# Performance work log

Measured on AMD Instinct MI355X. Metric: run time of the kernel, lower is better.

Reference implementation:

```python
import jax, jax.numpy as jnp
import numpy as np

# SSD300 common_params
MAP_SIZES = np.array([38, 19, 10, 5, 3, 1])
NUM_BOXES = np.array([4, 6, 6, 6, 4, 4])
NUM_OFFSET = 4
LOC_VAR = 0.1
NUM_CLASSES = 21
NEG_POS_RATIO = 3
_counts = MAP_SIZES ** 2 * NUM_BOXES
LAYER_OFFSETS = np.concatenate([[0], np.cumsum(_counts)])[:6]
TOTAL_ANCHORS = int(_counts.sum())  # 8732

B, MAXGT, SEG_HW = 32, 64, 300


def setup_inputs() -> dict:
    key = jax.random.key(0)
    ks = jax.random.split(key, 6)
    rng = np.random.default_rng(0)
    layer = rng.integers(0, 6, (B, MAXGT))
    pos = rng.integers(0, MAP_SIZES[layer] ** 2)
    dbox = rng.integers(0, NUM_BOXES[layer])
    nvalid = rng.integers(8, MAXGT + 1, (B,))
    live = np.arange(MAXGT)[None, :] < nvalid[:, None]
    layer = np.where(live, layer, -100)  # -100 sentinel terminates per-image list
    idx_batch = jnp.asarray(np.stack([np.zeros_like(layer), layer, pos, dbox], -1), dtype=jnp.int64)
    cls_batch = jnp.asarray(rng.integers(1, NUM_CLASSES, (B, MAXGT)), dtype=jnp.int64)
    return {
        "Loc": jax.random.normal(ks[0], (B, TOTAL_ANCHORS, NUM_OFFSET), jnp.float32),
        "Cls": jax.random.normal(ks[1], (B, TOTAL_ANCHORS, NUM_CLASSES), jnp.float32),
        "Seg": jax.random.normal(ks[2], (B, NUM_CLASSES, SEG_HW, SEG_HW), jnp.float32),
        "gt_box_batch": jax.random.uniform(ks[3], (B, MAXGT, NUM_OFFSET), jnp.float32),
        "df_box_batch": jax.random.uniform(ks[4], (B, MAXGT, NUM_OFFSET), jnp.float32),
        "idx_batch": idx_batch,
        "cls_batch": cls_batch,
        "bat_s": B,
        "mining": 1,
        "seg_label": jax.random.randint(ks[5], (B, SEG_HW, SEG_HW), 0, NUM_CLASSES, jnp.int64),
    }


def _build_targets(idx_batch, cls_batch, gt_box_batch, df_box_batch, mining):
    # Vectorized replacement of the nested scalar-scatter loop.
    layer = idx_batch[..., 1]
    fpos = idx_batch[..., 2]
    dbox = idx_batch[..., 3]
    # original loop breaks at first -100: mask everything after it
    valid = jnp.cumprod((layer != -100).astype(jnp.int32), axis=1).astype(bool)
    lc = jnp.clip(layer, 0, 5)
    offs = jnp.asarray(LAYER_OFFSETS)[lc]
    nb = jnp.asarray(NUM_BOXES)[lc]
    # [B, num_boxes, H, W] permuted to [B, H, W, num_boxes] -> flat = pos*nb + dbox
    flat = offs + fpos * nb + dbox
    flat = jnp.where(valid, flat, TOTAL_ANCHORS)  # dump slot
    bsz = idx_batch.shape[0]
    b_idx = jnp.arange(bsz)[:, None]
    init = -1 if mining else 0
    cls_t = jnp.full((bsz, TOTAL_ANCHORS + 1), init, dtype=jnp.int32)
    cls_t = cls_t.at[b_idx, flat].set(jnp.where(valid, cls_batch.astype(jnp.int32), init))
    delta = (gt_box_batch - df_box_batch) / LOC_VAR
    loc_t = jnp.zeros((bsz, TOTAL_ANCHORS + 1, NUM_OFFSET), jnp.float32)
    loc_t = loc_t.at[b_idx, flat].set(jnp.where(valid[..., None], delta, 0.0))
    return cls_t[:, :TOTAL_ANCHORS], loc_t[:, :TOTAL_ANCHORS]


def _mt_loss(Loc, Cls, Seg, gt_box_batch, df_box_batch, idx_batch, cls_batch, mining, seg_label):
    cls_t, loc_t = _build_targets(idx_batch, cls_batch, gt_box_batch, df_box_batch, mining)
    pos = cls_t > 0
    num_pos = jnp.maximum(pos.sum(), 1).astype(jnp.float32)
    logp = jax.nn.log_softmax(Cls, axis=-1)  # [B,N,C]
    ce = -jnp.take_along_axis(logp, jnp.clip(cls_t, 0, NUM_CLASSES - 1)[..., None].astype(jnp.int32), axis=-1)[..., 0]
    loss_cls_pos = jnp.where(pos, ce, 0.0).sum()
    if mining:
        # hard negative mining: top (3*num_pos_i) background losses per image
        ce_bg = -logp[..., 0]
        neg_cand = cls_t == -1
        scores = jnp.where(neg_cand, ce_bg, -jnp.inf)
        order = jnp.argsort(-scores, axis=1)
        rank = jnp.argsort(order, axis=1)
        num_pos_i = pos.sum(axis=1, keepdims=True)
        num_neg_i = jnp.minimum(NEG_POS_RATIO * num_pos_i, neg_cand.sum(axis=1, keepdims=True))
        sel = neg_cand & (rank < num_neg_i)
        loss_cls_neg = jnp.where(sel, ce_bg, 0.0).sum()
    else:
        # all non-positive anchors are explicit background targets (cls_t == 0)
        loss_cls_neg = jnp.where(~pos, ce, 0.0).sum()
    loss_cls = (loss_cls_pos + loss_cls_neg) / num_pos
    d = Loc - loc_t
    ad = jnp.abs(d)
    sl1 = jnp.where(ad < 1.0, 0.5 * d * d, ad - 0.5)
    loss_loc = jnp.where(pos[..., None], sl1, 0.0).sum() / num_pos
    seg_logp = jax.nn.log_softmax(Seg, axis=1)  # [B,C,H,W]
    seg_ce = -jnp.take_along_axis(seg_logp, seg_label[:, None].astype(jnp.int32), axis=1)[:, 0]
    loss_seg = seg_ce.mean()
    return loss_cls + loss_loc + loss_seg


def reference(Loc, Cls, Seg, gt_box_batch, df_box_batch, idx_batch, cls_batch, bat_s, mining, seg_label):
    return _mt_loss(Loc, Cls, Seg, gt_box_batch, df_box_batch, idx_batch, cls_batch, mining, seg_label)
```

## Files before the change

### kernel.cpp

```cpp
#include <hip/hip_runtime.h>
#include <stdint.h>

#define BATCH 32
#define NA 8732
#define NC 21
#define SHW 90000
#define MAXGT 64
#define NQ (SHW / 4)

#define SLABQ 512
#define NSLAB ((NQ + SLABQ - 1) / SLABQ)
#define NBLK (BATCH * NSLAB)

__constant__ int c_loff[6] = {0, 5776, 7942, 8542, 8692, 8728};
__constant__ int c_lnb[6]  = {4, 6, 6, 6, 4, 4};

__device__ __forceinline__ unsigned f2key(float f) {
    unsigned u = __float_as_uint(f);
    return (u & 0x80000000u) ? ~u : (u | 0x80000000u);
}
__device__ __forceinline__ float key2f(unsigned k) {
    return __uint_as_float((k & 0x80000000u) ? (k ^ 0x80000000u) : ~k);
}

__global__ __launch_bounds__(64) void k_init(float* __restrict__ acc, int* __restrict__ npt,
                                             unsigned* __restrict__ done) {
    int t = threadIdx.x;
    if (t < 8) acc[t] = 0.0f;
    if (t == 8) *npt = 0;
    if (t == 9) *done = 0u;
}

__global__ __launch_bounds__(1024) void k_build(
    const int* __restrict__ idxb, const int* __restrict__ clsb,
    const float* __restrict__ gt, const float* __restrict__ df,
    const float* __restrict__ Loc, const int* __restrict__ mining_p,
    signed char* __restrict__ cls_t, float* __restrict__ acc,
    int* __restrict__ num_pos_i, int* __restrict__ neg_cnt_i,
    int* __restrict__ npt)
{
    const int b = blockIdx.x;
    const int tid = threadIdx.x;
    __shared__ int s_flat[MAXGT];
    __shared__ int s_cls[MAXGT];
    __shared__ float s_delta[MAXGT][4];
    __shared__ int s_nv;
    __shared__ float s_wf[16];
    __shared__ int s_wp[16];
    __shared__ int s_wn[16];

    if (tid < MAXGT) {
        int layer = idxb[(b * MAXGT + tid) * 4 + 1];
        int fpos  = idxb[(b * MAXGT + tid) * 4 + 2];
        int dbox  = idxb[(b * MAXGT + tid) * 4 + 3];
        int fl;
        if (layer == -100) fl = -2;
        else {
            int lc = min(max(layer, 0), 5);
            fl = c_loff[lc] + fpos * c_lnb[lc] + dbox;
        }
        s_flat[tid] = fl;
        s_cls[tid] = clsb[b * MAXGT + tid];
        #pragma unroll
        for (int o = 0; o < 4; o++)
            s_delta[tid][o] = (gt[(b * MAXGT + tid) * 4 + o] - df[(b * MAXGT + tid) * 4 + o]) / 0.1f;
    }
    __syncthreads();
    if (tid == 0) {
        int nv = MAXGT;
        for (int j = 0; j < MAXGT; j++) if (s_flat[j] == -2) { nv = j; break; }
        s_nv = nv;
    }
    __syncthreads();
    const int nv = s_nv;

    int rflat[MAXGT];
    #pragma unroll
    for (int j = 0; j < MAXGT; j++)
        rflat[j] = (j < nv) ? s_flat[j] : -3;

    const int mining = *mining_p;
    const signed char cinit = mining ? (signed char)(-1) : (signed char)0;
    int pos_cnt = 0, neg_cnt = 0;
    float loc_sum = 0.0f;

    for (int a = tid; a < NA; a += 1024) {
        int best = -1;
        #pragma unroll
        for (int j = 0; j < MAXGT; j++)
            best = (rflat[j] == a) ? j : best;
        signed char cv = cinit;
        if (best >= 0) cv = (signed char)s_cls[best];
        cls_t[b * NA + a] = cv;
        if (cv > 0) {
            pos_cnt++;
            const float4 l4 = *reinterpret_cast<const float4*>(Loc + ((size_t)b * NA + a) * 4);
            float lv[4] = {l4.x, l4.y, l4.z, l4.w};
            #pragma unroll
            for (int o = 0; o < 4; o++) {
                float d = lv[o] - s_delta[best][o];
                float ad = fabsf(d);
                loc_sum += (ad < 1.0f) ? (0.5f * d * d) : (ad - 0.5f);
            }
        } else if (cv == -1) {
            neg_cnt++;
        }
    }

    #pragma unroll
    for (int d = 32; d > 0; d >>= 1) {
        loc_sum += __shfl_down(loc_sum, d);
        pos_cnt += __shfl_down(pos_cnt, d);
        neg_cnt += __shfl_down(neg_cnt, d);
    }
    const int lane = tid & 63, wv = tid >> 6;
    if (lane == 0) { s_wf[wv] = loc_sum; s_wp[wv] = pos_cnt; s_wn[wv] = neg_cnt; }
    __syncthreads();
    if (tid == 0) {
        float lf = 0.0f; int pp = 0, nn = 0;
        #pragma unroll
        for (int w = 0; w < 16; w++) { lf += s_wf[w]; pp += s_wp[w]; nn += s_wn[w]; }
        atomicAdd(acc + 2, lf);
        num_pos_i[b] = pp;
        atomicAdd(npt, pp);
        neg_cnt_i[b] = nn;
    }
}

__global__ __launch_bounds__(256) void k_cls(
    const float* __restrict__ Cls, const signed char* __restrict__ cls_t,
    const int* __restrict__ mining_p, float* __restrict__ scores,
    float* __restrict__ acc)
{
    __shared__ __align__(16) float s_c[256 * NC];
    __shared__ float s_wp[4];
    __shared__ float s_wn[4];
    const int t = threadIdx.x;
    const size_t base = (size_t)blockIdx.x * (256 * NC);
    const size_t total = (size_t)BATCH * NA * NC;
    const int nchunks = (int)((total - base) >> 2) < (256 * NC / 4)
                        ? (int)((total - base) >> 2) : (256 * NC / 4);
    #pragma unroll
    for (int k = 0; k < 6; k++) {
        int j4 = t + k * 256;
        if (j4 < nchunks) {
            *reinterpret_cast<float4*>(&s_c[j4 * 4]) =
                *reinterpret_cast<const float4*>(Cls + base + (size_t)j4 * 4);
        }
    }
    __syncthreads();

    const int r = blockIdx.x * 256 + t;
    const int mining = *mining_p;
    float pos_ce = 0.0f, neg_ce = 0.0f;
    if (r < BATCH * NA) {
        float f[NC];
        #pragma unroll
        for (int c = 0; c < NC; c++) f[c] = s_c[t * NC + c];
        float m = f[0];
        #pragma unroll
        for (int c = 1; c < NC; c++) m = fmaxf(m, f[c]);
        float s = 0.0f;
        #pragma unroll
        for (int c = 0; c < NC; c++) s += __expf(f[c] - m);
        float lse = m + __logf(s);
        int ct = (int)cls_t[r];
        int lab = ct > 0 ? ct : 0;
        float xt = f[0];
        #pragma unroll
        for (int c = 1; c < NC; c++) xt = (c == lab) ? f[c] : xt;
        float ce_bg = lse - f[0];
        if (ct > 0) pos_ce = lse - xt;
        if (mining) {
            scores[r] = (ct == -1) ? ce_bg : -__builtin_inff();
        } else if (ct <= 0) {
            neg_ce = ce_bg;
        }
    }
    #pragma unroll
    for (int d = 32; d > 0; d >>= 1) {
        pos_ce += __shfl_down(pos_ce, d);
        neg_ce += __shfl_down(neg_ce, d);
    }
    const int lane = t & 63, wv = t >> 6;
    if (lane == 0) { s_wp[wv] = pos_ce; s_wn[wv] = neg_ce; }
    __syncthreads();
    if (t == 0) {
        float p = s_wp[0] + s_wp[1] + s_wp[2] + s_wp[3];
        float n = s_wn[0] + s_wn[1] + s_wn[2] + s_wn[3];
        if (p != 0.0f) atomicAdd(acc + 0, p);
        if (n != 0.0f) atomicAdd(acc + 1, n);
    }
}

__global__ __launch_bounds__(256) void k_topk(
    const float* __restrict__ scores, const int* __restrict__ num_pos_i,
    const int* __restrict__ neg_cnt_i, const int* __restrict__ mining_p,
    float* __restrict__ acc)
{
    if (*mining_p == 0) return;
    const int b = blockIdx.x;
    const int tid = threadIdx.x;
    const int k = min(3 * num_pos_i[b], neg_cnt_i[b]);
    if (k <= 0) return;

    __shared__ unsigned s_keys[NA];
    __shared__ int s_hist[256];
    __shared__ int s_wsum[4];
    __shared__ int s_selb;
    __shared__ int s_sele;
    __shared__ float s_wf[4];
    __shared__ int s_wc[4];

    const float* sc = scores + (size_t)b * NA;
    for (int a = tid; a < NA; a += 256)
        s_keys[a] = f2key(sc[a]);

    const int lane = tid & 63, wv = tid >> 6;
    unsigned pref = 0u;
    int k_rem = k;

    #pragma unroll
    for (int lvl = 0; lvl < 4; lvl++) {
        const int sh = 24 - lvl * 8;
        s_hist[tid] = 0;
        __syncthreads();
        for (int a = tid; a < NA; a += 256) {
            unsigned key = s_keys[a];
            bool in = (lvl == 0) || ((key >> (sh + 8)) == pref);
            if (in) atomicAdd(&s_hist[(key >> sh) & 0xFF], 1);
        }
        __syncthreads();
        const int b_rev = 255 - tid;
        const int v = s_hist[b_rev];
        int x = v;
        #pragma unroll
        for (int d = 1; d < 64; d <<= 1) {
            int o = __shfl_up(x, d);
            if (lane >= d) x += o;
        }
        if (lane == 63) s_wsum[wv] = x;
        __syncthreads();
        for (int w = 0; w < wv; w++) x += s_wsum[w];
        if (x >= k_rem && (x - v) < k_rem) { s_selb = b_rev; s_sele = x - v; }
        __syncthreads();
        pref = (pref << 8) | (unsigned)s_selb;
        k_rem -= s_sele;
        __syncthreads();
    }

    float sum_g = 0.0f; int cnt_g = 0;
    for (int a = tid; a < NA; a += 256) {
        unsigned key = s_keys[a];
        if (key > pref) { sum_g += key2f(key); cnt_g++; }
    }
    #pragma unroll
    for (int d = 32; d > 0; d >>= 1) {
        sum_g += __shfl_down(sum_g, d);
        cnt_g += __shfl_down(cnt_g, d);
    }
    if (lane == 0) { s_wf[wv] = sum_g; s_wc[wv] = cnt_g; }
    __syncthreads();
    if (tid == 0) {
        float sg = s_wf[0] + s_wf[1] + s_wf[2] + s_wf[3];
        int cg = s_wc[0] + s_wc[1] + s_wc[2] + s_wc[3];
        atomicAdd(acc + 1, sg + (float)(k - cg) * key2f(pref));
    }
}

__device__ __forceinline__ void upd1(float& m, float& s, float& tg,
                                     int lab, float x, int c) {
    tg = (lab == c) ? x : tg;
    const float d = x - m;
    const float e = __expf(-fabsf(d));
    s = (d > 0.0f) ? fmaf(s, e, 1.0f) : (s + e);
    m = fmaxf(m, x);
}
__device__ __forceinline__ void upd4(float4& m, float4& s, float4& tg,
                                     const int4& lab, const float4& x, int c) {
    upd1(m.x, s.x, tg.x, lab.x, x.x, c);
    upd1(m.y, s.y, tg.y, lab.y, x.y, c);
    upd1(m.z, s.z, tg.z, lab.z, x.z, c);
    upd1(m.w, s.w, tg.w, lab.w, x.w, c);
}

#define GLOAD_F4(dst, addr) \
    asm volatile("global_load_dwordx4 %0, %1, off" : "=v"(dst) : "v"(addr))
#define GLOAD_I4(dst, addr) \
    asm volatile("global_load_dwordx4 %0, %1, off" : "=v"(dst) : "v"(addr))
#define SWAIT(lit) do { \
    asm volatile("s_waitcnt vmcnt(" #lit ")" ::: "memory"); \
    __builtin_amdgcn_sched_barrier(0); } while (0)

__global__ __launch_bounds__(256) void k_seg(
    const float* __restrict__ Seg, const int* __restrict__ slab_lab,
    float* __restrict__ acc, const int* __restrict__ npt,
    unsigned* __restrict__ done, float* __restrict__ out)
{
    __shared__ float s_w[4];
    const int t = threadIdx.x;
    const int img = blockIdx.x / NSLAB;
    const int sl  = blockIdx.x - img * NSLAB;
    const int qbase = sl * SLABQ;
    const int q0 = qbase + t;
    const int q1 = qbase + 256 + t;
    const bool vb = (q1 < NQ);
    const int q1s = vb ? q1 : q0;

    const float4* segq = (const float4*)(Seg + (size_t)img * NC * SHW);
    const int4* labq = (const int4*)(slab_lab + (size_t)img * SHW);

    const uint64_t abase = (uint64_t)(segq + q0);
    const uint64_t bbase = (uint64_t)(segq + q1s);
    const uint64_t cstep = (uint64_t)NQ * 16;

    int4 la, lb;
    float4 A0, A1, B0, B1;

    GLOAD_I4(la, (uint64_t)(labq + q0));
    GLOAD_I4(lb, (uint64_t)(labq + q1s));
    GLOAD_F4(A0, abase);
    GLOAD_F4(B0, bbase);
    GLOAD_F4(A1, abase + cstep);
    GLOAD_F4(B1, bbase + cstep);

    SWAIT(4);

    float4 ma, sa, ta, mb, sb, tb;
    bool init = false;

    #pragma unroll
    for (int c = 0; c < NC - 1; ++c) {
        SWAIT(2);
        const float4 xa = (c & 1) ? A1 : A0;
        const float4 xb = (c & 1) ? B1 : B0;
        if (!init) {
            ma = xa; ta = xa; mb = xb; tb = xb;
            sa = make_float4(1.f, 1.f, 1.f, 1.f);
            sb = make_float4(1.f, 1.f, 1.f, 1.f);
            init = true;
        } else {
            upd4(ma, sa, ta, la, xa, c);
            upd4(mb, sb, tb, lb, xb, c);
        }
        if (c + 2 < NC) {
            const uint64_t off = (uint64_t)(c + 2) * cstep;
            if (c & 1) { GLOAD_F4(A1, abase + off); GLOAD_F4(B1, bbase + off); }
            else       { GLOAD_F4(A0, abase + off); GLOAD_F4(B0, bbase + off); }
        }
    }
    SWAIT(0);
    upd4(ma, sa, ta, la, A0, NC - 1);
    upd4(mb, sb, tb, lb, B0, NC - 1);

    float lsum = (ma.x + __logf(sa.x) - ta.x)
               + (ma.y + __logf(sa.y) - ta.y)
               + (ma.z + __logf(sa.z) - ta.z)
               + (ma.w + __logf(sa.w) - ta.w);
    if (vb) {
        lsum += (mb.x + __logf(sb.x) - tb.x)
              + (mb.y + __logf(sb.y) - tb.y)
              + (mb.z + __logf(sb.z) - tb.z)
              + (mb.w + __logf(sb.w) - tb.w);
    }

    #pragma unroll
    for (int d = 32; d > 0; d >>= 1) lsum += __shfl_down(lsum, d);
    const int lane = t & 63, wv = t >> 6;
    if (lane == 0) s_w[wv] = lsum;
    __syncthreads();
    if (t == 0) {
        atomicAdd(acc + 3, s_w[0] + s_w[1] + s_w[2] + s_w[3]);
        __threadfence();
        unsigned old = atomicAdd(done, 1u);
        if (old == gridDim.x - 1) {
            __threadfence();
            int np_i = *npt;
            float np = (float)(np_i > 1 ? np_i : 1);
            out[0] = (acc[0] + acc[1] + acc[2]) / np
                   + acc[3] / (float)(BATCH * SHW);
        }
    }
}

extern "C" void kernel_launch(void* const* d_in, const int* in_sizes, int n_in,
                              void* d_out, int out_size, void* d_ws, size_t ws_size,
                              hipStream_t stream)
{
    const float* Loc = (const float*)d_in[0];
    const float* Cls = (const float*)d_in[1];
    const float* Seg = (const float*)d_in[2];
    const float* gt  = (const float*)d_in[3];
    const float* df  = (const float*)d_in[4];
    const int* idxb  = (const int*)d_in[5];
    const int* clsb  = (const int*)d_in[6];
    const int* mining_p = (const int*)d_in[8];
    const int* slab  = (const int*)d_in[9];
    float* out = (float*)d_out;

    char* ws = (char*)d_ws;
    float* acc        = (float*)ws;
    int*   npt        = (int*)(ws + 32);
    unsigned* done    = (unsigned*)(ws + 36);
    int*   num_pos_i  = (int*)(ws + 64);
    int*   neg_cnt_i  = (int*)(ws + 192);
    signed char* cls_t = (signed char*)(ws + 512);
    float* scores      = (float*)(ws + 512 + 279424);

    hipLaunchKernelGGL(k_init, dim3(1), dim3(64), 0, stream, acc, npt, done);
    hipLaunchKernelGGL(k_build, dim3(BATCH), dim3(1024), 0, stream,
                       idxb, clsb, gt, df, Loc, mining_p, cls_t, acc, num_pos_i, neg_cnt_i, npt);
    hipLaunchKernelGGL(k_cls, dim3((BATCH * NA + 255) / 256), dim3(256), 0, stream,
                       Cls, cls_t, mining_p, scores, acc);
    hipLaunchKernelGGL(k_topk, dim3(BATCH), dim3(256), 0, stream,
                       scores, num_pos_i, neg_cnt_i, mining_p, acc);
    hipLaunchKernelGGL(k_seg, dim3(NBLK), dim3(256), 0, stream,
                       Seg, slab, acc, npt, done, out);
}
```

Baseline: 143.1 us.

## Fuse target build, class CE and top-k mining into one per-image kernel

Merges the init, target-build, class cross-entropy and hard-negative top-k kernels into one kernel with one 1024-thread block per image. Class targets stay in registers and mining scores go straight into shared memory, so the cls_t and scores round trips to global memory, three launches and the global atomics all disappear. Per-image partial sums go to workspace and are summed by the last segmentation block. The segmentation kernel also moves from double to triple buffering of its class-plane loads. The risk is that the Cls read (about 23 MB) is now handled by only 32 blocks with uncoalesced per-row loads, instead of being spread across the whole GPU.

```diff
diff --git a/kernel.cpp b/kernel.cpp
--- a/kernel.cpp
+++ b/kernel.cpp
@@ -23,31 +23,32 @@
     return __uint_as_float((k & 0x80000000u) ? (k ^ 0x80000000u) : ~k);
 }
 
-__global__ __launch_bounds__(64) void k_init(float* __restrict__ acc, int* __restrict__ npt,
-                                             unsigned* __restrict__ done) {
-    int t = threadIdx.x;
-    if (t < 8) acc[t] = 0.0f;
-    if (t == 8) *npt = 0;
-    if (t == 9) *done = 0u;
-}
-
-__global__ __launch_bounds__(1024) void k_build(
+__global__ __launch_bounds__(1024) void k_front(
     const int* __restrict__ idxb, const int* __restrict__ clsb,
     const float* __restrict__ gt, const float* __restrict__ df,
-    const float* __restrict__ Loc, const int* __restrict__ mining_p,
-    signed char* __restrict__ cls_t, float* __restrict__ acc,
-    int* __restrict__ num_pos_i, int* __restrict__ neg_cnt_i,
-    int* __restrict__ npt)
+    const float* __restrict__ Loc, const float* __restrict__ Cls,
+    const int* __restrict__ mining_p,
+    float* __restrict__ loc_i, float* __restrict__ posce_i,
+    float* __restrict__ negce_i, int* __restrict__ np_i,
+    float* __restrict__ segacc, unsigned* __restrict__ done)
 {
     const int b = blockIdx.x;
     const int tid = threadIdx.x;
+    if (b == 0 && tid == 0) { *segacc = 0.0f; *done = 0u; }
+
     __shared__ int s_flat[MAXGT];
     __shared__ int s_cls[MAXGT];
     __shared__ float s_delta[MAXGT][4];
     __shared__ int s_nv;
-    __shared__ float s_wf[16];
-    __shared__ int s_wp[16];
-    __shared__ int s_wn[16];
+    __shared__ float s_rf[16];
+    __shared__ float s_rf2[16];
+    __shared__ int s_ri[16];
+    __shared__ int s_ri2[16];
+    __shared__ int s_pp, s_nn;
+    __shared__ unsigned s_keys[NA];
+    __shared__ int s_hist[256];
+    __shared__ int s_wsum[4];
+    __shared__ int s_selb, s_sele;
 
     if (tid < MAXGT) {
         int layer = idxb[(b * MAXGT + tid) * 4 + 1];
@@ -67,9 +68,9 @@
     }
     __syncthreads();
     if (tid == 0) {
-        int nv = MAXGT;
-        for (int j = 0; j < MAXGT; j++) if (s_flat[j] == -2) { nv = j; break; }
-        s_nv = nv;
+        int nvv = MAXGT;
+        for (int j = 0; j < MAXGT; j++) if (s_flat[j] == -2) { nvv = j; break; }
+        s_nv = nvv;
     }
     __syncthreads();
     const int nv = s_nv;
@@ -81,30 +82,35 @@
 
     const int mining = *mining_p;
     const signed char cinit = mining ? (signed char)(-1) : (signed char)0;
+
+    signed char cvr[9];
     int pos_cnt = 0, neg_cnt = 0;
     float loc_sum = 0.0f;
-
-    for (int a = tid; a < NA; a += 1024) {
-        int best = -1;
-        #pragma unroll
-        for (int j = 0; j < MAXGT; j++)
-            best = (rflat[j] == a) ? j : best;
+    #pragma unroll
+    for (int i = 0; i < 9; i++) {
+        const int a = tid + i * 1024;
         signed char cv = cinit;
-        if (best >= 0) cv = (signed char)s_cls[best];
-        cls_t[b * NA + a] = cv;
-        if (cv > 0) {
-            pos_cnt++;
-            const float4 l4 = *reinterpret_cast<const float4*>(Loc + ((size_t)b * NA + a) * 4);
-            float lv[4] = {l4.x, l4.y, l4.z, l4.w};
-            #pragma unroll
-            for (int o = 0; o < 4; o++) {
-                float d = lv[o] - s_delta[best][o];
-                float ad = fabsf(d);
-                loc_sum += (ad < 1.0f) ? (0.5f * d * d) : (ad - 0.5f);
-            }
-        } else if (cv == -1) {
-            neg_cnt++;
-        }
+        if (a < NA) {
+            int best = -1;
+            #pragma unroll
+            for (int j = 0; j < MAXGT; j++)
+                best = (rflat[j] == a) ? j : best;
+            if (best >= 0) cv = (signed char)s_cls[best];
+            if (cv > 0) {
+                pos_cnt++;
+                const float4 l4 = *reinterpret_cast<const float4*>(Loc + ((size_t)b * NA + a) * 4);
+                float lv[4] = {l4.x, l4.y, l4.z, l4.w};
+                #pragma unroll
+                for (int o = 0; o < 4; o++) {
+                    float d = lv[o] - s_delta[best][o];
+                    float ad = fabsf(d);
+                    loc_sum += (ad < 1.0f) ? (0.5f * d * d) : (ad - 0.5f);
+                }
+            } else if (cv == -1) {
+                neg_cnt++;
+            }
+        }
+        cvr[i] = cv;
     }
 
     #pragma unroll
@@ -114,159 +120,129 @@
         neg_cnt += __shfl_down(neg_cnt, d);
     }
     const int lane = tid & 63, wv = tid >> 6;
-    if (lane == 0) { s_wf[wv] = loc_sum; s_wp[wv] = pos_cnt; s_wn[wv] = neg_cnt; }
+    if (lane == 0) { s_rf[wv] = loc_sum; s_ri[wv] = pos_cnt; s_ri2[wv] = neg_cnt; }
     __syncthreads();
     if (tid == 0) {
         float lf = 0.0f; int pp = 0, nn = 0;
         #pragma unroll
-        for (int w = 0; w < 16; w++) { lf += s_wf[w]; pp += s_wp[w]; nn += s_wn[w]; }
-        atomicAdd(acc + 2, lf);
-        num_pos_i[b] = pp;
-        atomicAdd(npt, pp);
-        neg_cnt_i[b] = nn;
-    }
-}
-
-__global__ __launch_bounds__(256) void k_cls(
-    const float* __restrict__ Cls, const signed char* __restrict__ cls_t,
-    const int* __restrict__ mining_p, float* __restrict__ scores,
-    float* __restrict__ acc)
-{
-    __shared__ __align__(16) float s_c[256 * NC];
-    __shared__ float s_wp[4];
-    __shared__ float s_wn[4];
-    const int t = threadIdx.x;
-    const size_t base = (size_t)blockIdx.x * (256 * NC);
-    const size_t total = (size_t)BATCH * NA * NC;
-    const int nchunks = (int)((total - base) >> 2) < (256 * NC / 4)
-                        ? (int)((total - base) >> 2) : (256 * NC / 4);
-    #pragma unroll
-    for (int k = 0; k < 6; k++) {
-        int j4 = t + k * 256;
-        if (j4 < nchunks) {
-            *reinterpret_cast<float4*>(&s_c[j4 * 4]) =
-                *reinterpret_cast<const float4*>(Cls + base + (size_t)j4 * 4);
-        }
-    }
-    __syncthreads();
-
-    const int r = blockIdx.x * 256 + t;
-    const int mining = *mining_p;
+        for (int w = 0; w < 16; w++) { lf += s_rf[w]; pp += s_ri[w]; nn += s_ri2[w]; }
+        loc_i[b] = lf;
+        np_i[b] = pp;
+        s_pp = pp; s_nn = nn;
+    }
+    __syncthreads();
+
+    const float* clsrow = Cls + (size_t)b * NA * NC;
     float pos_ce = 0.0f, neg_ce = 0.0f;
-    if (r < BATCH * NA) {
-        float f[NC];
-        #pragma unroll
-        for (int c = 0; c < NC; c++) f[c] = s_c[t * NC + c];
-        float m = f[0];
-        #pragma unroll
-        for (int c = 1; c < NC; c++) m = fmaxf(m, f[c]);
-        float s = 0.0f;
-        #pragma unroll
-        for (int c = 0; c < NC; c++) s += __expf(f[c] - m);
-        float lse = m + __logf(s);
-        int ct = (int)cls_t[r];
-        int lab = ct > 0 ? ct : 0;
-        float xt = f[0];
-        #pragma unroll
-        for (int c = 1; c < NC; c++) xt = (c == lab) ? f[c] : xt;
-        float ce_bg = lse - f[0];
-        if (ct > 0) pos_ce = lse - xt;
-        if (mining) {
-            scores[r] = (ct == -1) ? ce_bg : -__builtin_inff();
-        } else if (ct <= 0) {
-            neg_ce = ce_bg;
-        }
-    }
+    #pragma unroll
+    for (int i = 0; i < 9; i++) {
+        const int r = tid + i * 1024;
+        if (r < NA) {
+            const float* row = clsrow + (size_t)r * NC;
+            float f[NC];
+            #pragma unroll
+            for (int c = 0; c < NC; c++) f[c] = row[c];
+            float m = f[0];
+            #pragma unroll
+            for (int c = 1; c < NC; c++) m = fmaxf(m, f[c]);
+            float s = 0.0f;
+            #pragma unroll
+            for (int c = 0; c < NC; c++) s += __expf(f[c] - m);
+            float lse = m + __logf(s);
+            int ct = (int)cvr[i];
+            int lab = ct > 0 ? ct : 0;
+            float xt = f[0];
+            #pragma unroll
+            for (int c = 1; c < NC; c++) xt = (c == lab) ? f[c] : xt;
+            float ce_bg = lse - f[0];
+            if (ct > 0) pos_ce += lse - xt;
+            if (mining) {
+                s_keys[r] = f2key((ct == -1) ? ce_bg : -__builtin_inff());
+            } else if (ct <= 0) {
+                neg_ce += ce_bg;
+            }
+        }
+    }
+
+    float pc = pos_ce, ncv = neg_ce;
     #pragma unroll
     for (int d = 32; d > 0; d >>= 1) {
-        pos_ce += __shfl_down(pos_ce, d);
-        neg_ce += __shfl_down(neg_ce, d);
-    }
-    const int lane = t & 63, wv = t >> 6;
-    if (lane == 0) { s_wp[wv] = pos_ce; s_wn[wv] = neg_ce; }
-    __syncthreads();
-    if (t == 0) {
-        float p = s_wp[0] + s_wp[1] + s_wp[2] + s_wp[3];
-        float n = s_wn[0] + s_wn[1] + s_wn[2] + s_wn[3];
-        if (p != 0.0f) atomicAdd(acc + 0, p);
-        if (n != 0.0f) atomicAdd(acc + 1, n);
-    }
-}
-
-__global__ __launch_bounds__(256) void k_topk(
-    const float* __restrict__ scores, const int* __restrict__ num_pos_i,
-    const int* __restrict__ neg_cnt_i, const int* __restrict__ mining_p,
-    float* __restrict__ acc)
-{
-    if (*mining_p == 0) return;
-    const int b = blockIdx.x;
-    const int tid = threadIdx.x;
-    const int k = min(3 * num_pos_i[b], neg_cnt_i[b]);
-    if (k <= 0) return;
-
-    __shared__ unsigned s_keys[NA];
-    __shared__ int s_hist[256];
-    __shared__ int s_wsum[4];
-    __shared__ int s_selb;
-    __shared__ int s_sele;
-    __shared__ float s_wf[4];
-    __shared__ int s_wc[4];
-
-    const float* sc = scores + (size_t)b * NA;
-    for (int a = tid; a < NA; a += 256)
-        s_keys[a] = f2key(sc[a]);
-
-    const int lane = tid & 63, wv = tid >> 6;
-    unsigned pref = 0u;
-    int k_rem = k;
-
-    #pragma unroll
-    for (int lvl = 0; lvl < 4; lvl++) {
-        const int sh = 24 - lvl * 8;
-        s_hist[tid] = 0;
+        pc += __shfl_down(pc, d);
+        ncv += __shfl_down(ncv, d);
+    }
+    if (lane == 0) { s_rf[wv] = pc; s_rf2[wv] = ncv; }
+    __syncthreads();
+    if (tid == 0) {
+        float p = 0.0f, n = 0.0f;
+        #pragma unroll
+        for (int w = 0; w < 16; w++) { p += s_rf[w]; n += s_rf2[w]; }
+        posce_i[b] = p;
+        if (!mining) negce_i[b] = n;
+    }
+
+    if (mining) {
+        const int k = min(3 * s_pp, s_nn);
+        if (k <= 0) {
+            if (tid == 0) negce_i[b] = 0.0f;
+            return;
+        }
+        unsigned pref = 0u;
+        int k_rem = k;
+        #pragma unroll
+        for (int lvl = 0; lvl < 4; lvl++) {
+            const int sh = 24 - lvl * 8;
+            if (tid < 256) s_hist[tid] = 0;
+            __syncthreads();
+            for (int a = tid; a < NA; a += 1024) {
+                unsigned key = s_keys[a];
+                bool in = (lvl == 0) || ((key >> (sh + 8)) == pref);
+                if (in) atomicAdd(&s_hist[(key >> sh) & 0xFF], 1);
+            }
+            __syncthreads();
+            int v = 0, x = 0, b_rev = 0;
+            if (tid < 256) {
+                b_rev = 255 - tid;
+                v = s_hist[b_rev];
+                x = v;
+                #pragma unroll
+                for (int d = 1; d < 64; d <<= 1) {
+                    int o = __shfl_up(x, d);
+                    if (lane >= d) x += o;
+                }
+                if (lane == 63) s_wsum[wv] = x;
+            }
+            __syncthreads();
+            if (tid < 256) {
+                for (int w = 0; w < wv; w++) x += s_wsum[w];
+                if (x >= k_rem && (x - v) < k_rem) { s_selb = b_rev; s_sele = x - v; }
+            }
+            __syncthreads();
+            pref = (pref << 8) | (unsigned)s_selb;
+            k_rem -= s_sele;
+            __syncthreads();
+        }
+
+        float sum_g = 0.0f; int cnt_g = 0;
+        for (int a = tid; a < NA; a += 1024) {
+            unsigned key = s_keys[a];
+            if (key > pref) { sum_g += key2f(key); cnt_g++; }
+        }
+        #pragma unroll
+        for (int d = 32; d > 0; d >>= 1) {
+            sum_g += __shfl_down(sum_g, d);
+            cnt_g += __shfl_down(cnt_g, d);
+        }
+        if (lane == 0) { s_rf[wv] = sum_g; s_ri[wv] = cnt_g; }
         __syncthreads();
-        for (int a = tid; a < NA; a += 256) {
-            unsigned key = s_keys[a];
-            bool in = (lvl == 0) || ((key >> (sh + 8)) == pref);
-            if (in) atomicAdd(&s_hist[(key >> sh) & 0xFF], 1);
-        }
-        __syncthreads();
-        const int b_rev = 255 - tid;
-        const int v = s_hist[b_rev];
-        int x = v;
-        #pragma unroll
-        for (int d = 1; d < 64; d <<= 1) {
-            int o = __shfl_up(x, d);
-            if (lane >= d) x += o;
-        }
-        if (lane == 63) s_wsum[wv] = x;
-        __syncthreads();
-        for (int w = 0; w < wv; w++) x += s_wsum[w];
-        if (x >= k_rem && (x - v) < k_rem) { s_selb = b_rev; s_sele = x - v; }
-        __syncthreads();
-        pref = (pref << 8) | (unsigned)s_selb;
-        k_rem -= s_sele;
-        __syncthreads();
-    }
-
-    float sum_g = 0.0f; int cnt_g = 0;
-    for (int a = tid; a < NA; a += 256) {
-        unsigned key = s_keys[a];
-        if (key > pref) { sum_g += key2f(key); cnt_g++; }
-    }
-    #pragma unroll
-    for (int d = 32; d > 0; d >>= 1) {
-        sum_g += __shfl_down(sum_g, d);
-        cnt_g += __shfl_down(cnt_g, d);
-    }
-    if (lane == 0) { s_wf[wv] = sum_g; s_wc[wv] = cnt_g; }
-    __syncthreads();
-    if (tid == 0) {
-        float sg = s_wf[0] + s_wf[1] + s_wf[2] + s_wf[3];
-        int cg = s_wc[0] + s_wc[1] + s_wc[2] + s_wc[3];
-        atomicAdd(acc + 1, sg + (float)(k - cg) * key2f(pref));
-    }
-}
+        if (tid == 0) {
+            float sg = 0.0f; int cg = 0;
+            #pragma unroll
+            for (int w = 0; w < 16; w++) { sg += s_rf[w]; cg += s_ri[w]; }
+            negce_i[b] = sg + (float)(k - cg) * key2f(pref);
+        }
+    }
+}
+
 
 __device__ __forceinline__ void upd1(float& m, float& s, float& tg,
                                      int lab, float x, int c) {
@@ -294,8 +270,10 @@
 
 __global__ __launch_bounds__(256) void k_seg(
     const float* __restrict__ Seg, const int* __restrict__ slab_lab,
-    float* __restrict__ acc, const int* __restrict__ npt,
-    unsigned* __restrict__ done, float* __restrict__ out)
+    float* __restrict__ segacc, const int* __restrict__ np_i,
+    const float* __restrict__ loc_i, const float* __restrict__ posce_i,
+    const float* __restrict__ negce_i, unsigned* __restrict__ done,
+    float* __restrict__ out)
 {
     __shared__ float s_w[4];
     const int t = threadIdx.x;
@@ -315,43 +293,41 @@
     const uint64_t cstep = (uint64_t)NQ * 16;
 
     int4 la, lb;
-    float4 A0, A1, B0, B1;
+    float4 A0, A1, A2, B0, B1, B2;
 
     GLOAD_I4(la, (uint64_t)(labq + q0));
     GLOAD_I4(lb, (uint64_t)(labq + q1s));
-    GLOAD_F4(A0, abase);
-    GLOAD_F4(B0, bbase);
-    GLOAD_F4(A1, abase + cstep);
-    GLOAD_F4(B1, bbase + cstep);
-
-    SWAIT(4);
+    GLOAD_F4(A0, abase);                 GLOAD_F4(B0, bbase);
+    GLOAD_F4(A1, abase + cstep);         GLOAD_F4(B1, bbase + cstep);
+    GLOAD_F4(A2, abase + 2 * cstep);     GLOAD_F4(B2, bbase + 2 * cstep);
+
+    SWAIT(6);
 
     float4 ma, sa, ta, mb, sb, tb;
-    bool init = false;
-
-    #pragma unroll
-    for (int c = 0; c < NC - 1; ++c) {
-        SWAIT(2);
-        const float4 xa = (c & 1) ? A1 : A0;
-        const float4 xb = (c & 1) ? B1 : B0;
-        if (!init) {
+
+    #pragma unroll
+    for (int c = 0; c < NC; ++c) {
+        if (c == NC - 1)      SWAIT(0);
+        else if (c == NC - 2) SWAIT(2);
+        else                  SWAIT(4);
+        const int sl3 = c % 3;
+        const float4 xa = (sl3 == 0) ? A0 : ((sl3 == 1) ? A1 : A2);
+        const float4 xb = (sl3 == 0) ? B0 : ((sl3 == 1) ? B1 : B2);
+        if (c == 0) {
             ma = xa; ta = xa; mb = xb; tb = xb;
             sa = make_float4(1.f, 1.f, 1.f, 1.f);
             sb = make_float4(1.f, 1.f, 1.f, 1.f);
-            init = true;
         } else {
             upd4(ma, sa, ta, la, xa, c);
             upd4(mb, sb, tb, lb, xb, c);
         }
-        if (c + 2 < NC) {
-            const uint64_t off = (uint64_t)(c + 2) * cstep;
-            if (c & 1) { GLOAD_F4(A1, abase + off); GLOAD_F4(B1, bbase + off); }
-            else       { GLOAD_F4(A0, abase + off); GLOAD_F4(B0, bbase + off); }
-        }
-    }
-    SWAIT(0);
-    upd4(ma, sa, ta, la, A0, NC - 1);
-    upd4(mb, sb, tb, lb, B0, NC - 1);
+        if (c + 3 < NC) {
+            const uint64_t off = (uint64_t)(c + 3) * cstep;
+            if (sl3 == 0)      { GLOAD_F4(A0, abase + off); GLOAD_F4(B0, bbase + off); }
+            else if (sl3 == 1) { GLOAD_F4(A1, abase + off); GLOAD_F4(B1, bbase + off); }
+            else               { GLOAD_F4(A2, abase + off); GLOAD_F4(B2, bbase + off); }
+        }
+    }
 
     float lsum = (ma.x + __logf(sa.x) - ta.x)
                + (ma.y + __logf(sa.y) - ta.y)
@@ -366,19 +342,22 @@
 
     #pragma unroll
     for (int d = 32; d > 0; d >>= 1) lsum += __shfl_down(lsum, d);
-    const int lane = t & 63, wv = t >> 6;
-    if (lane == 0) s_w[wv] = lsum;
+    const int lane = t & 63, wvv = t >> 6;
+    if (lane == 0) s_w[wvv] = lsum;
     __syncthreads();
     if (t == 0) {
-        atomicAdd(acc + 3, s_w[0] + s_w[1] + s_w[2] + s_w[3]);
+        atomicAdd(segacc, s_w[0] + s_w[1] + s_w[2] + s_w[3]);
         __threadfence();
         unsigned old = atomicAdd(done, 1u);
         if (old == gridDim.x - 1) {
             __threadfence();
-            int np_i = *npt;
-            float np = (float)(np_i > 1 ? np_i : 1);
-            out[0] = (acc[0] + acc[1] + acc[2]) / np
-                   + acc[3] / (float)(BATCH * SHW);
+            int np = 0; float lc = 0.0f, pcs = 0.0f, ncs = 0.0f;
+            #pragma unroll
+            for (int i = 0; i < BATCH; i++) {
+                np += np_i[i]; lc += loc_i[i]; pcs += posce_i[i]; ncs += negce_i[i];
+            }
+            float npf = (float)(np > 1 ? np : 1);
+            out[0] = (pcs + ncs + lc) / npf + (*segacc) / (float)(BATCH * SHW);
         }
     }
 }
@@ -399,21 +378,16 @@
     float* out = (float*)d_out;
 
     char* ws = (char*)d_ws;
-    float* acc        = (float*)ws;
-    int*   npt        = (int*)(ws + 32);
-    unsigned* done    = (unsigned*)(ws + 36);
-    int*   num_pos_i  = (int*)(ws + 64);
-    int*   neg_cnt_i  = (int*)(ws + 192);
-    signed char* cls_t = (signed char*)(ws + 512);
-    float* scores      = (float*)(ws + 512 + 279424);
-
-    hipLaunchKernelGGL(k_init, dim3(1), dim3(64), 0, stream, acc, npt, done);
-    hipLaunchKernelGGL(k_build, dim3(BATCH), dim3(1024), 0, stream,
-                       idxb, clsb, gt, df, Loc, mining_p, cls_t, acc, num_pos_i, neg_cnt_i, npt);
-    hipLaunchKernelGGL(k_cls, dim3((BATCH * NA + 255) / 256), dim3(256), 0, stream,
-                       Cls, cls_t, mining_p, scores, acc);
-    hipLaunchKernelGGL(k_topk, dim3(BATCH), dim3(256), 0, stream,
-                       scores, num_pos_i, neg_cnt_i, mining_p, acc);
+    float* segacc     = (float*)ws;
+    unsigned* done    = (unsigned*)(ws + 4);
+    int*   np_i       = (int*)(ws + 64);
+    float* loc_i      = (float*)(ws + 192);
+    float* posce_i    = (float*)(ws + 320);
+    float* negce_i    = (float*)(ws + 448);
+
+    hipLaunchKernelGGL(k_front, dim3(BATCH), dim3(1024), 0, stream,
+                       idxb, clsb, gt, df, Loc, Cls, mining_p,
+                       loc_i, posce_i, negce_i, np_i, segacc, done);
     hipLaunchKernelGGL(k_seg, dim3(NBLK), dim3(256), 0, stream,
-                       Seg, slab, acc, npt, done, out);
-}
+                       Seg, slab, segacc, np_i, loc_i, posce_i, negce_i, done, out);
+}
```

After: 155.6 us. 8.7% more time.

## Stage Seg channels through LDS with async global-to-LDS triple buffering

Applied to the files above, without the earlier changes.

The segmentation kernel now launches 256 persistent-style blocks (8 per image), each owning 2816 quads. Channels are streamed into a three-slot LDS ring with direct global-to-LDS loads, and each thread keeps 11 quads of online-softmax state in registers. Labels are packed into bytes to save registers. This is meant to get more memory requests in flight per CU and to cut per-block launch and tail overhead. In exchange it runs at only one block per CU with heavy LDS use, and it adds a block barrier on every channel.

```diff
diff --git a/kernel.cpp b/kernel.cpp
--- a/kernel.cpp
+++ b/kernel.cpp
@@ -8,9 +8,12 @@
 #define MAXGT 64
 #define NQ (SHW / 4)
 
-#define SLABQ 512
-#define NSLAB ((NQ + SLABQ - 1) / SLABQ)
-#define NBLK (BATCH * NSLAB)
+#define SPI 8
+#define SQUADS 2816
+#define QPT 11
+#define WQ 704
+#define CHBF (SQUADS * 4)
+#define CSTEP ((size_t)NQ * 16)
 
 __constant__ int c_loff[6] = {0, 5776, 7942, 8542, 8692, 8728};
 __constant__ int c_lnb[6]  = {4, 6, 6, 6, 4, 4};
@@ -268,6 +271,7 @@
     }
 }
 
+
 __device__ __forceinline__ void upd1(float& m, float& s, float& tg,
                                      int lab, float x, int c) {
     tg = (lab == c) ? x : tg;
@@ -276,98 +280,118 @@
     s = (d > 0.0f) ? fmaf(s, e, 1.0f) : (s + e);
     m = fmaxf(m, x);
 }
-__device__ __forceinline__ void upd4(float4& m, float4& s, float4& tg,
-                                     const int4& lab, const float4& x, int c) {
-    upd1(m.x, s.x, tg.x, lab.x, x.x, c);
-    upd1(m.y, s.y, tg.y, lab.y, x.y, c);
-    upd1(m.z, s.z, tg.z, lab.z, x.z, c);
-    upd1(m.w, s.w, tg.w, lab.w, x.w, c);
-}
-
-#define GLOAD_F4(dst, addr) \
-    asm volatile("global_load_dwordx4 %0, %1, off" : "=v"(dst) : "v"(addr))
+__device__ __forceinline__ void upd4p(float4& m, float4& s, float4& tg,
+                                      unsigned lp, const float4& x, int c) {
+    upd1(m.x, s.x, tg.x, (int)(lp & 0xFFu),         x.x, c);
+    upd1(m.y, s.y, tg.y, (int)((lp >> 8) & 0xFFu),  x.y, c);
+    upd1(m.z, s.z, tg.z, (int)((lp >> 16) & 0xFFu), x.z, c);
+    upd1(m.w, s.w, tg.w, (int)((lp >> 24) & 0xFFu), x.w, c);
+}
+
 #define GLOAD_I4(dst, addr) \
     asm volatile("global_load_dwordx4 %0, %1, off" : "=v"(dst) : "v"(addr))
 #define SWAIT(lit) do { \
     asm volatile("s_waitcnt vmcnt(" #lit ")" ::: "memory"); \
     __builtin_amdgcn_sched_barrier(0); } while (0)
 
-__global__ __launch_bounds__(256) void k_seg(
+__device__ __forceinline__ void stage_chan(const char* segbase, int c,
+                                           float* ldswave, const uint32_t* boff) {
+    const char* cb = segbase + (size_t)c * CSTEP;
+    #pragma unroll
+    for (int i = 0; i < QPT; i++) {
+        __builtin_amdgcn_global_load_lds(
+            (__attribute__((address_space(1))) void*)(cb + boff[i]),
+            (__attribute__((address_space(3))) void*)(ldswave + i * 256),
+            16, 0, 0);
+    }
+}
+
+#define RBAR() do { \
+    __builtin_amdgcn_sched_barrier(0); \
+    __builtin_amdgcn_s_barrier(); \
+    __builtin_amdgcn_sched_barrier(0); } while (0)
+
+__global__ __launch_bounds__(256, 1) void k_seg(
     const float* __restrict__ Seg, const int* __restrict__ slab_lab,
     float* __restrict__ acc, const int* __restrict__ npt,
     unsigned* __restrict__ done, float* __restrict__ out)
 {
+    __shared__ __align__(16) float s_buf[3 * CHBF];
     __shared__ float s_w[4];
     const int t = threadIdx.x;
-    const int img = blockIdx.x / NSLAB;
-    const int sl  = blockIdx.x - img * NSLAB;
-    const int qbase = sl * SLABQ;
-    const int q0 = qbase + t;
-    const int q1 = qbase + 256 + t;
-    const bool vb = (q1 < NQ);
-    const int q1s = vb ? q1 : q0;
-
-    const float4* segq = (const float4*)(Seg + (size_t)img * NC * SHW);
-    const int4* labq = (const int4*)(slab_lab + (size_t)img * SHW);
-
-    const uint64_t abase = (uint64_t)(segq + q0);
-    const uint64_t bbase = (uint64_t)(segq + q1s);
-    const uint64_t cstep = (uint64_t)NQ * 16;
-
-    int4 la, lb;
-    float4 A0, A1, B0, B1;
-
-    GLOAD_I4(la, (uint64_t)(labq + q0));
-    GLOAD_I4(lb, (uint64_t)(labq + q1s));
-    GLOAD_F4(A0, abase);
-    GLOAD_F4(B0, bbase);
-    GLOAD_F4(A1, abase + cstep);
-    GLOAD_F4(B1, bbase + cstep);
-
-    SWAIT(4);
-
-    float4 ma, sa, ta, mb, sb, tb;
-    bool init = false;
-
-    #pragma unroll
-    for (int c = 0; c < NC - 1; ++c) {
-        SWAIT(2);
-        const float4 xa = (c & 1) ? A1 : A0;
-        const float4 xb = (c & 1) ? B1 : B0;
-        if (!init) {
-            ma = xa; ta = xa; mb = xb; tb = xb;
-            sa = make_float4(1.f, 1.f, 1.f, 1.f);
-            sb = make_float4(1.f, 1.f, 1.f, 1.f);
-            init = true;
-        } else {
-            upd4(ma, sa, ta, la, xa, c);
-            upd4(mb, sb, tb, lb, xb, c);
-        }
-        if (c + 2 < NC) {
-            const uint64_t off = (uint64_t)(c + 2) * cstep;
-            if (c & 1) { GLOAD_F4(A1, abase + off); GLOAD_F4(B1, bbase + off); }
-            else       { GLOAD_F4(A0, abase + off); GLOAD_F4(B0, bbase + off); }
-        }
+    const int lane = t & 63, w = t >> 6;
+    const int img = blockIdx.x >> 3;
+    const int sl  = blockIdx.x & 7;
+    const int qbase = sl * SQUADS;
+
+    const char* segbase = (const char*)(Seg + (size_t)img * NC * SHW);
+    const char* labbase = (const char*)(slab_lab + (size_t)img * SHW);
+
+    int4 la[QPT];
+    #pragma unroll
+    for (int k = 0; k < QPT; k++) {
+        int q = qbase + t + k * 256;
+        int qc = (q < NQ) ? q : (NQ - 1);
+        GLOAD_I4(la[k], (uint64_t)labbase + (uint64_t)qc * 16u);
     }
     SWAIT(0);
-    upd4(ma, sa, ta, la, A0, NC - 1);
-    upd4(mb, sb, tb, lb, B0, NC - 1);
-
-    float lsum = (ma.x + __logf(sa.x) - ta.x)
-               + (ma.y + __logf(sa.y) - ta.y)
-               + (ma.z + __logf(sa.z) - ta.z)
-               + (ma.w + __logf(sa.w) - ta.w);
-    if (vb) {
-        lsum += (mb.x + __logf(sb.x) - tb.x)
-              + (mb.y + __logf(sb.y) - tb.y)
-              + (mb.z + __logf(sb.z) - tb.z)
-              + (mb.w + __logf(sb.w) - tb.w);
+    unsigned lp[QPT];
+    #pragma unroll
+    for (int k = 0; k < QPT; k++)
+        lp[k] = ((unsigned)la[k].x & 0xFFu) | (((unsigned)la[k].y & 0xFFu) << 8)
+              | (((unsigned)la[k].z & 0xFFu) << 16) | (((unsigned)la[k].w & 0xFFu) << 24);
+
+    uint32_t boff[QPT];
+    #pragma unroll
+    for (int i = 0; i < QPT; i++) {
+        int qg = qbase + w * WQ + i * 64 + lane;
+        int qc = (qg < NQ) ? qg : (NQ - 1);
+        boff[i] = (uint32_t)qc * 16u;
+    }
+    float* ldsw0 = s_buf + (size_t)w * (WQ * 4);
+
+    float4 m4[QPT], s4[QPT], t4[QPT];
+
+    stage_chan(segbase, 0, ldsw0, boff);
+    stage_chan(segbase, 1, ldsw0 + CHBF, boff);
+    SWAIT(11);
+    RBAR();
+    stage_chan(segbase, 2, ldsw0 + 2 * CHBF, boff);
+    #pragma unroll
+    for (int k = 0; k < QPT; k++) {
+        float4 x = *reinterpret_cast<const float4*>(s_buf + (size_t)(t + k * 256) * 4);
+        m4[k] = x; t4[k] = x;
+        s4[k] = make_float4(1.f, 1.f, 1.f, 1.f);
+    }
+
+    #pragma unroll 1
+    for (int c = 1; c < NC; ++c) {
+        if (c == NC - 1) SWAIT(0); else SWAIT(11);
+        RBAR();
+        if (c + 2 < NC) stage_chan(segbase, c + 2, ldsw0 + ((c + 2) % 3) * CHBF, boff);
+        const float* bp = s_buf + (size_t)(c % 3) * CHBF;
+        #pragma unroll
+        for (int k = 0; k < QPT; k++) {
+            float4 x = *reinterpret_cast<const float4*>(bp + (size_t)(t + k * 256) * 4);
+            upd4p(m4[k], s4[k], t4[k], lp[k], x, c);
+        }
+    }
+
+    float lsum = 0.0f;
+    #pragma unroll
+    for (int k = 0; k < QPT; k++) {
+        int q = qbase + t + k * 256;
+        if (q < NQ) {
+            lsum += (m4[k].x + __logf(s4[k].x) - t4[k].x)
+                  + (m4[k].y + __logf(s4[k].y) - t4[k].y)
+                  + (m4[k].z + __logf(s4[k].z) - t4[k].z)
+                  + (m4[k].w + __logf(s4[k].w) - t4[k].w);
+        }
     }
 
     #pragma unroll
     for (int d = 32; d > 0; d >>= 1) lsum += __shfl_down(lsum, d);
-    const int lane = t & 63, wv = t >> 6;
-    if (lane == 0) s_w[wv] = lsum;
+    if (lane == 0) s_w[w] = lsum;
     __syncthreads();
     if (t == 0) {
         atomicAdd(acc + 3, s_w[0] + s_w[1] + s_w[2] + s_w[3]);
@@ -414,6 +438,6 @@
                        Cls, cls_t, mining_p, scores, acc);
     hipLaunchKernelGGL(k_topk, dim3(BATCH), dim3(256), 0, stream,
                        scores, num_pos_i, neg_cnt_i, mining_p, acc);
-    hipLaunchKernelGGL(k_seg, dim3(NBLK), dim3(256), 0, stream,
+    hipLaunchKernelGGL(k_seg, dim3(BATCH * SPI), dim3(256), 0, stream,
                        Seg, slab, acc, npt, done, out);
 }
```

Measured after the change: 124.5 us. 13.0% less time.

## Split segmentation CE into channel-group exp-sum pass and log reduction pass

Applied to the files above, without the earlier changes.

Replaces the single-pass online max/log-sum-exp segmentation kernel with two kernels. The first splits channels into two groups and pixels into four regions per image, and sums plain exp values held in registers. It writes the partial sums to workspace and accumulates target logits separately. The second kernel adds the two partial sums and takes the log. This drops the max tracking and the branchy online update, but it loses numerical stability for large logits, adds extra workspace write/read traffic, and runs at low occupancy of one block per CU with no load/compute overlap across channels.

```diff
diff --git a/kernel.cpp b/kernel.cpp
--- a/kernel.cpp
+++ b/kernel.cpp
@@ -8,9 +8,9 @@
 #define MAXGT 64
 #define NQ (SHW / 4)
 
-#define SLABQ 512
-#define NSLAB ((NQ + SLABQ - 1) / SLABQ)
-#define NBLK (BATCH * NSLAB)
+#define P_PX 22500
+#define P_Q  5625
+#define ITR  22
 
 __constant__ int c_loff[6] = {0, 5776, 7942, 8542, 8692, 8728};
 __constant__ int c_lnb[6]  = {4, 6, 6, 6, 4, 4};
@@ -268,102 +268,110 @@
     }
 }
 
-__device__ __forceinline__ void upd1(float& m, float& s, float& tg,
-                                     int lab, float x, int c) {
-    tg = (lab == c) ? x : tg;
-    const float d = x - m;
-    const float e = __expf(-fabsf(d));
-    s = (d > 0.0f) ? fmaf(s, e, 1.0f) : (s + e);
-    m = fmaxf(m, x);
-}
-__device__ __forceinline__ void upd4(float4& m, float4& s, float4& tg,
-                                     const int4& lab, const float4& x, int c) {
-    upd1(m.x, s.x, tg.x, lab.x, x.x, c);
-    upd1(m.y, s.y, tg.y, lab.y, x.y, c);
-    upd1(m.z, s.z, tg.z, lab.z, x.z, c);
-    upd1(m.w, s.w, tg.w, lab.w, x.w, c);
-}
-
-#define GLOAD_F4(dst, addr) \
-    asm volatile("global_load_dwordx4 %0, %1, off" : "=v"(dst) : "v"(addr))
-#define GLOAD_I4(dst, addr) \
-    asm volatile("global_load_dwordx4 %0, %1, off" : "=v"(dst) : "v"(addr))
-#define SWAIT(lit) do { \
-    asm volatile("s_waitcnt vmcnt(" #lit ")" ::: "memory"); \
-    __builtin_amdgcn_sched_barrier(0); } while (0)
-
-__global__ __launch_bounds__(256) void k_seg(
+__global__ __launch_bounds__(256, 1) void k_seg1(
     const float* __restrict__ Seg, const int* __restrict__ slab_lab,
+    float* __restrict__ ws0, float* __restrict__ ws1,
+    float* __restrict__ acc)
+{
+    __shared__ float s_w[4];
+    const int t = threadIdx.x;
+    const int g = blockIdx.x & 1;
+    const int r = (blockIdx.x >> 1) & 3;
+    const int b = blockIdx.x >> 3;
+    const int c0 = g ? 11 : 0;
+    const int c1 = g ? 21 : 11;
+
+    const int4* labq = (const int4*)(slab_lab + (size_t)b * SHW + (size_t)r * P_PX);
+    unsigned lp[ITR];
+    #pragma unroll
+    for (int i = 0; i < ITR; i++) {
+        int q = t + i * 256;
+        int4 la = (q < P_Q) ? labq[q] : make_int4(255, 255, 255, 255);
+        lp[i] = ((unsigned)la.x & 0xFFu) | (((unsigned)la.y & 0xFFu) << 8)
+              | (((unsigned)la.z & 0xFFu) << 16) | (((unsigned)la.w & 0xFFu) << 24);
+    }
+
+    float4 acc4[ITR];
+    float tsum = 0.0f;
+
+    #pragma unroll 1
+    for (int c = c0; c < c1; ++c) {
+        const float4* cp = (const float4*)(Seg + ((size_t)(b * NC + c)) * SHW
+                                               + (size_t)r * P_PX);
+        float4 xx[ITR];
+        #pragma unroll
+        for (int i = 0; i < ITR; i++) {
+            int q = t + i * 256;
+            if (q < P_Q) xx[i] = cp[q];
+        }
+        if (c == c0) {
+            #pragma unroll
+            for (int i = 0; i < ITR; i++) {
+                int q = t + i * 256;
+                if (q < P_Q) {
+                    const float4 x = xx[i];
+                    const unsigned l = lp[i];
+                    tsum += ((l         & 0xFFu) == (unsigned)c) ? x.x : 0.0f;
+                    tsum += (((l >> 8)  & 0xFFu) == (unsigned)c) ? x.y : 0.0f;
+                    tsum += (((l >> 16) & 0xFFu) == (unsigned)c) ? x.z : 0.0f;
+                    tsum += (((l >> 24) & 0xFFu) == (unsigned)c) ? x.w : 0.0f;
+                    acc4[i] = make_float4(__expf(x.x), __expf(x.y),
+                                          __expf(x.z), __expf(x.w));
+                }
+            }
+        } else {
+            #pragma unroll
+            for (int i = 0; i < ITR; i++) {
+                int q = t + i * 256;
+                if (q < P_Q) {
+                    const float4 x = xx[i];
+                    const unsigned l = lp[i];
+                    tsum += ((l         & 0xFFu) == (unsigned)c) ? x.x : 0.0f;
+                    tsum += (((l >> 8)  & 0xFFu) == (unsigned)c) ? x.y : 0.0f;
+                    tsum += (((l >> 16) & 0xFFu) == (unsigned)c) ? x.z : 0.0f;
+                    tsum += (((l >> 24) & 0xFFu) == (unsigned)c) ? x.w : 0.0f;
+                    acc4[i].x += __expf(x.x);
+                    acc4[i].y += __expf(x.y);
+                    acc4[i].z += __expf(x.z);
+                    acc4[i].w += __expf(x.w);
+                }
+            }
+        }
+    }
+
+    float* wsp = g ? ws1 : ws0;
+    float4* wp = (float4*)wsp + (size_t)b * (SHW / 4) + (size_t)r * P_Q;
+    #pragma unroll
+    for (int i = 0; i < ITR; i++) {
+        int q = t + i * 256;
+        if (q < P_Q) wp[q] = acc4[i];
+    }
+
+    #pragma unroll
+    for (int d = 32; d > 0; d >>= 1) tsum += __shfl_down(tsum, d);
+    const int lane = t & 63, wv = t >> 6;
+    if (lane == 0) s_w[wv] = tsum;
+    __syncthreads();
+    if (t == 0) atomicAdd(acc + 4, s_w[0] + s_w[1] + s_w[2] + s_w[3]);
+}
+
+__global__ __launch_bounds__(256) void k_seg2(
+    const float* __restrict__ ws0, const float* __restrict__ ws1,
     float* __restrict__ acc, const int* __restrict__ npt,
     unsigned* __restrict__ done, float* __restrict__ out)
 {
     __shared__ float s_w[4];
     const int t = threadIdx.x;
-    const int img = blockIdx.x / NSLAB;
-    const int sl  = blockIdx.x - img * NSLAB;
-    const int qbase = sl * SLABQ;
-    const int q0 = qbase + t;
-    const int q1 = qbase + 256 + t;
-    const bool vb = (q1 < NQ);
-    const int q1s = vb ? q1 : q0;
-
-    const float4* segq = (const float4*)(Seg + (size_t)img * NC * SHW);
-    const int4* labq = (const int4*)(slab_lab + (size_t)img * SHW);
-
-    const uint64_t abase = (uint64_t)(segq + q0);
-    const uint64_t bbase = (uint64_t)(segq + q1s);
-    const uint64_t cstep = (uint64_t)NQ * 16;
-
-    int4 la, lb;
-    float4 A0, A1, B0, B1;
-
-    GLOAD_I4(la, (uint64_t)(labq + q0));
-    GLOAD_I4(lb, (uint64_t)(labq + q1s));
-    GLOAD_F4(A0, abase);
-    GLOAD_F4(B0, bbase);
-    GLOAD_F4(A1, abase + cstep);
-    GLOAD_F4(B1, bbase + cstep);
-
-    SWAIT(4);
-
-    float4 ma, sa, ta, mb, sb, tb;
-    bool init = false;
-
-    #pragma unroll
-    for (int c = 0; c < NC - 1; ++c) {
-        SWAIT(2);
-        const float4 xa = (c & 1) ? A1 : A0;
-        const float4 xb = (c & 1) ? B1 : B0;
-        if (!init) {
-            ma = xa; ta = xa; mb = xb; tb = xb;
-            sa = make_float4(1.f, 1.f, 1.f, 1.f);
-            sb = make_float4(1.f, 1.f, 1.f, 1.f);
-            init = true;
-        } else {
-            upd4(ma, sa, ta, la, xa, c);
-            upd4(mb, sb, tb, lb, xb, c);
-        }
-        if (c + 2 < NC) {
-            const uint64_t off = (uint64_t)(c + 2) * cstep;
-            if (c & 1) { GLOAD_F4(A1, abase + off); GLOAD_F4(B1, bbase + off); }
-            else       { GLOAD_F4(A0, abase + off); GLOAD_F4(B0, bbase + off); }
-        }
-    }
-    SWAIT(0);
-    upd4(ma, sa, ta, la, A0, NC - 1);
-    upd4(mb, sb, tb, lb, B0, NC - 1);
-
-    float lsum = (ma.x + __logf(sa.x) - ta.x)
-               + (ma.y + __logf(sa.y) - ta.y)
-               + (ma.z + __logf(sa.z) - ta.z)
-               + (ma.w + __logf(sa.w) - ta.w);
-    if (vb) {
-        lsum += (mb.x + __logf(sb.x) - tb.x)
-              + (mb.y + __logf(sb.y) - tb.y)
-              + (mb.z + __logf(sb.z) - tb.z)
-              + (mb.w + __logf(sb.w) - tb.w);
-    }
-
+    const int N4 = BATCH * SHW / 4;
+    const float4* p0 = (const float4*)ws0;
+    const float4* p1 = (const float4*)ws1;
+    float lsum = 0.0f;
+    for (int j = blockIdx.x * 256 + t; j < N4; j += 256 * 256) {
+        const float4 a = p0[j];
+        const float4 b = p1[j];
+        lsum += __logf(a.x + b.x) + __logf(a.y + b.y)
+              + __logf(a.z + b.z) + __logf(a.w + b.w);
+    }
     #pragma unroll
     for (int d = 32; d > 0; d >>= 1) lsum += __shfl_down(lsum, d);
     const int lane = t & 63, wv = t >> 6;
@@ -378,7 +386,7 @@
             int np_i = *npt;
             float np = (float)(np_i > 1 ? np_i : 1);
             out[0] = (acc[0] + acc[1] + acc[2]) / np
-                   + acc[3] / (float)(BATCH * SHW);
+                   + (acc[3] - acc[4]) / (float)(BATCH * SHW);
         }
     }
 }
@@ -406,6 +414,8 @@
     int*   neg_cnt_i  = (int*)(ws + 192);
     signed char* cls_t = (signed char*)(ws + 512);
     float* scores      = (float*)(ws + 512 + 279424);
+    float* ws0         = (float*)(ws + (size_t)2  * 1024 * 1024);
+    float* ws1         = (float*)(ws + (size_t)16 * 1024 * 1024);
 
     hipLaunchKernelGGL(k_init, dim3(1), dim3(64), 0, stream, acc, npt, done);
     hipLaunchKernelGGL(k_build, dim3(BATCH), dim3(1024), 0, stream,
@@ -414,6 +424,8 @@
                        Cls, cls_t, mining_p, scores, acc);
     hipLaunchKernelGGL(k_topk, dim3(BATCH), dim3(256), 0, stream,
                        scores, num_pos_i, neg_cnt_i, mining_p, acc);
-    hipLaunchKernelGGL(k_seg, dim3(NBLK), dim3(256), 0, stream,
-                       Seg, slab, acc, npt, done, out);
-}
+    hipLaunchKernelGGL(k_seg1, dim3(256), dim3(256), 0, stream,
+                       Seg, slab, ws0, ws1, acc);
+    hipLaunchKernelGGL(k_seg2, dim3(256), dim3(256), 0, stream,
+                       ws0, ws1, acc, npt, done, out);
+}
```

New measurement: 130.4 us. -8.9%, faster.
